# Kernel tuning notes

Measured on AMD Instinct MI355X. Metric: run time of the kernel, lower is better.

The kernel has to match this reference:

```python
import jax, jax.numpy as jnp
import numpy as np

N = 8192
DEGREE = 32          # fixed out-degree -> nnz(adj) = N*DEGREE, static for jit
NEG_SLOPE = 0.2      # GATConv default leaky_relu slope


def _gat_conv(x, src, dst, w, att_src, att_dst, b):
    """PyG GATConv (concat=True): x:[N,Fin], w:[Fin,H*C], att_*:[H,C], b:[H*C]."""
    n = x.shape[0]
    H, C = att_src.shape
    xl = (x @ w).reshape(n, H, C)                       # [N,H,C]
    a_s = jnp.einsum('nhc,hc->nh', xl, att_src)         # [N,H]
    a_d = jnp.einsum('nhc,hc->nh', xl, att_dst)         # [N,H]
    e = a_s[src] + a_d[dst]                             # [E,H]
    e = jnp.where(e > 0, e, NEG_SLOPE * e)              # leaky_relu
    # segment softmax over edges grouped by destination node
    m = jax.ops.segment_max(e, dst, num_segments=n)     # [N,H]
    ex = jnp.exp(e - m[dst])
    s = jax.ops.segment_sum(ex, dst, num_segments=n)    # [N,H]
    alpha = ex / s[dst]                                 # [E,H]
    out = jax.ops.segment_sum(alpha[:, :, None] * xl[src], dst, num_segments=n)
    return out.reshape(n, H * C) + b, alpha


def setup_inputs() -> dict:
    IN, HID, OUT, H = 256, 128, 64, 8
    key = jax.random.key(0)
    ks = jax.random.split(key, 12)

    x = jax.random.normal(ks[0], (N, IN), jnp.float32)

    # regular adjacency: node i -> (i+o) % N for o in 1..DEGREE (exactly N*DEGREE nonzeros)
    rows = jnp.repeat(jnp.arange(N), DEGREE)
    cols = ((jnp.arange(N)[:, None] + jnp.arange(1, DEGREE + 1)[None, :]) % N).reshape(-1)
    adj = jnp.zeros((N, N), jnp.float32).at[rows, cols].set(1.0)

    def glorot(k, shape):
        fan_in = shape[0] if len(shape) > 1 else shape[0]
        return jax.random.normal(k, shape, jnp.float32) * np.float32(1.0 / np.sqrt(fan_in))

    inp = {
        'x': x, 'adj': adj,
        'emb_w': glorot(ks[1], (IN, HID)), 'emb_b': jnp.zeros((HID,), jnp.float32),
        'w1': glorot(ks[2], (HID, H * HID)),
        'att_src1': jax.random.normal(ks[3], (H, HID), jnp.float32) * 0.1,
        'att_dst1': jax.random.normal(ks[4], (H, HID), jnp.float32) * 0.1,
        'b1': jnp.zeros((H * HID,), jnp.float32),
        'w2': glorot(ks[5], (H * HID, H * OUT)),
        'att_src2': jax.random.normal(ks[6], (H, OUT), jnp.float32) * 0.1,
        'att_dst2': jax.random.normal(ks[7], (H, OUT), jnp.float32) * 0.1,
        'b2': jnp.zeros((H * OUT,), jnp.float32),
    }
    return inp


def reference(x, adj, emb_w, emb_b, w1, att_src1, att_dst1, b1,
              w2, att_src2, att_dst2, b2):
    n = adj.shape[0]
    # dense_to_sparse: static nnz = N*DEGREE (by construction of adj)
    src, dst = jnp.nonzero(adj, size=n * DEGREE)
    h = x @ emb_w + emb_b                       # self.emb (dropout = identity in eval)
    h, _ = _gat_conv(h, src, dst, w1, att_src1, att_dst1, b1)
    h = jax.nn.relu(h)
    h, att = _gat_conv(h, src, dst, w2, att_src2, att_dst2, b2)
    h = jax.nn.relu(h)
    return h, att
```

## Files before the change

### kernel.cpp

```cpp
#include <hip/hip_runtime.h>
#include <hip/hip_bf16.h>

#define NN 8192
#define DEG 32

#define AS1 __attribute__((address_space(1)))
#define AS3 __attribute__((address_space(3)))

typedef unsigned short ushort_t;
typedef __attribute__((ext_vector_type(8))) short bf16x8;
typedef __attribute__((ext_vector_type(4))) float f32x4;

__device__ inline float bf_raw(unsigned short u) {
  return __uint_as_float(((unsigned int)u) << 16);
}
__device__ inline unsigned short f32_to_bf16_bits(float f) {
  __hip_bfloat16 b = __float2bfloat16(f);
  unsigned short u;
  __builtin_memcpy(&u, &b, sizeof(u));
  return u;
}
__device__ inline unsigned int pack2bf(float a, float b) {
  return (unsigned int)f32_to_bf16_bits(a) |
         ((unsigned int)f32_to_bf16_bits(b) << 16);
}

__device__ inline int detect_bf16(const unsigned int* __restrict__ raw) {
  __shared__ int s_cnt[4];
  int t = threadIdx.x;
  unsigned int w = raw[t];
  unsigned short lo = (unsigned short)(w & 0xffffu);
  int e = (lo >> 7) & 0xff;
  int ok = (lo == 0) || (e >= 96 && e <= 131);
  unsigned long long b = __ballot(ok);
  if ((t & 63) == 0) s_cnt[t >> 6] = __popcll(b);
  __syncthreads();
  int cnt = s_cnt[0] + s_cnt[1] + s_cnt[2] + s_cnt[3];
  __syncthreads();
  return cnt >= 145;
}

__device__ inline void tile_transpose64(const void* __restrict__ src,
                                        ushort_t* __restrict__ dst, int R,
                                        int C, int r0, int c0, int bf) {
  __shared__ float tile[64][65];
  int t = threadIdx.x;
  int cc = t & 63, rr = t >> 6;
#pragma unroll
  for (int p = 0; p < 16; ++p) {
    int r = p * 4 + rr;
    float v = bf ? bf_raw(((const ushort_t*)src)[(size_t)(r0 + r) * C + c0 + cc])
                 : ((const float*)src)[(size_t)(r0 + r) * C + c0 + cc];
    tile[r][cc] = v;
  }
  __syncthreads();
#pragma unroll
  for (int p = 0; p < 16; ++p) {
    int i = p * 4 + rr;
    dst[(size_t)(c0 + i) * R + r0 + cc] = f32_to_bf16_bits(tile[cc][i]);
  }
}

struct PrepArgs {
  const void* w2_raw;
  const void* embw_raw;
  const void* w1_raw;
  const void* embb_raw;
  ushort_t* w2t;
  ushort_t* W12t;
  float* b12;
  int* bfflag;
  const unsigned int* det;
};

__global__ __launch_bounds__(256) void prep_kernel(PrepArgs a) {
  int bf = detect_bf16(a.det);
  int b = blockIdx.x, t = threadIdx.x;
  if (b == 0 && t == 0) *a.bfflag = bf;
  if (b < 128) {
    tile_transpose64(a.w2_raw, a.w2t, 1024, 512, (b >> 3) * 64, (b & 7) * 64,
                     bf);
  } else {
    __shared__ float wcol[4][128];
    __shared__ float ebb[128];
    int idx = b - 128;
    int n0 = idx * 4;
    for (int i = t; i < 512; i += 256) {
      int n = i >> 7, j = i & 127;
      wcol[n][j] =
          bf ? bf_raw(((const ushort_t*)a.w1_raw)[(size_t)j * 1024 + n0 + n])
             : ((const float*)a.w1_raw)[(size_t)j * 1024 + n0 + n];
    }
    if (t < 128)
      ebb[t] = bf ? bf_raw(((const ushort_t*)a.embb_raw)[t])
                  : ((const float*)a.embb_raw)[t];
    __syncthreads();
    int k = t;
    float acc0 = 0.f, acc1 = 0.f, acc2 = 0.f, acc3 = 0.f;
#pragma unroll 4
    for (int jc = 0; jc < 16; ++jc) {
      float v[8];
      if (bf) {
        ushort4 u0 = ((const ushort4*)a.embw_raw)[k * 32 + jc * 2];
        ushort4 u1 = ((const ushort4*)a.embw_raw)[k * 32 + jc * 2 + 1];
        v[0] = bf_raw(u0.x); v[1] = bf_raw(u0.y);
        v[2] = bf_raw(u0.z); v[3] = bf_raw(u0.w);
        v[4] = bf_raw(u1.x); v[5] = bf_raw(u1.y);
        v[6] = bf_raw(u1.z); v[7] = bf_raw(u1.w);
      } else {
        float4 f0 = ((const float4*)a.embw_raw)[k * 32 + jc * 2];
        float4 f1 = ((const float4*)a.embw_raw)[k * 32 + jc * 2 + 1];
        v[0] = f0.x; v[1] = f0.y; v[2] = f0.z; v[3] = f0.w;
        v[4] = f1.x; v[5] = f1.y; v[6] = f1.z; v[7] = f1.w;
      }
#pragma unroll
      for (int jj = 0; jj < 8; ++jj) {
        acc0 = fmaf(v[jj], wcol[0][jc * 8 + jj], acc0);
        acc1 = fmaf(v[jj], wcol[1][jc * 8 + jj], acc1);
        acc2 = fmaf(v[jj], wcol[2][jc * 8 + jj], acc2);
        acc3 = fmaf(v[jj], wcol[3][jc * 8 + jj], acc3);
      }
    }
    a.W12t[(size_t)(n0 + 0) * 256 + k] = f32_to_bf16_bits(acc0);
    a.W12t[(size_t)(n0 + 1) * 256 + k] = f32_to_bf16_bits(acc1);
    a.W12t[(size_t)(n0 + 2) * 256 + k] = f32_to_bf16_bits(acc2);
    a.W12t[(size_t)(n0 + 3) * 256 + k] = f32_to_bf16_bits(acc3);
    int wv = t >> 6, ln = t & 63;
    float s = fmaf(ebb[ln], wcol[wv][ln], ebb[ln + 64] * wcol[wv][ln + 64]);
#pragma unroll
    for (int m = 1; m <= 32; m <<= 1) s += __shfl_xor(s, m);
    if (ln == 0) a.b12[n0 + wv] = s;
  }
}

template <int HPB, bool BIAS, bool ACHECK>
__global__ __launch_bounds__(512) void gemm_bt(
    const void* __restrict__ Araw, const ushort_t* __restrict__ Bt,
    const float* __restrict__ bias, ushort_t* __restrict__ C,
    const void* __restrict__ atts_raw, const void* __restrict__ attd_raw,
    float* __restrict__ a_s, float* __restrict__ a_d,
    const int* __restrict__ bfflag, int M, int N, int K) {
  __shared__ ushort_t As[128 * 64];
  __shared__ ushort_t Bs[128 * 64];
  __shared__ float ps[4][128], pd[4][128];
  int bf = bfflag[0];
  int abf = ACHECK ? bf : 1;
  int t = threadIdx.x;
  int wave = t >> 6, lane = t & 63;
  int wr = wave >> 2, wc = wave & 3;
  int wm = wr * 64, wn = wc * 32;
  int row0 = blockIdx.y * 128, col0 = blockIdx.x * 128;
  int q = lane >> 4, lr = lane & 15;
  int srow = t >> 3;
  int schunk = t & 7;

  int sc = (schunk ^ (srow & 7)) * 8;
  const ushort_t* gA0 = (const ushort_t*)Araw + (size_t)(row0 + srow) * K + sc;
  const ushort_t* gA1 =
      (const ushort_t*)Araw + (size_t)(row0 + 64 + srow) * K + sc;
  const float* fA0 = (const float*)Araw + (size_t)(row0 + srow) * K + sc;
  const float* fA1 = (const float*)Araw + (size_t)(row0 + 64 + srow) * K + sc;
  const ushort_t* gB0 = Bt + (size_t)(col0 + srow) * K + sc;
  const ushort_t* gB1 = Bt + (size_t)(col0 + 64 + srow) * K + sc;
  ushort_t* lA0 = As + srow * 64 + schunk * 8;
  ushort_t* lA1 = As + (64 + srow) * 64 + schunk * 8;
  ushort_t* lB0 = Bs + srow * 64 + schunk * 8;
  ushort_t* lB1 = Bs + (64 + srow) * 64 + schunk * 8;

  f32x4 acc[4][2];
#pragma unroll
  for (int i = 0; i < 4; ++i)
#pragma unroll
    for (int j = 0; j < 2; ++j)
#pragma unroll
      for (int r = 0; r < 4; ++r) acc[i][j][r] = 0.f;

  for (int k0 = 0; k0 < K; k0 += 64) {
    if (abf) {
      __builtin_amdgcn_global_load_lds((const AS1 void*)(gA0 + k0),
                                       (AS3 void*)lA0, 16, 0, 0);
      __builtin_amdgcn_global_load_lds((const AS1 void*)(gA1 + k0),
                                       (AS3 void*)lA1, 16, 0, 0);
    } else {
      float4 u0 = *(const float4*)(fA0 + k0);
      float4 u1 = *(const float4*)(fA0 + k0 + 4);
      uint4 o;
      o.x = pack2bf(u0.x, u0.y);
      o.y = pack2bf(u0.z, u0.w);
      o.z = pack2bf(u1.x, u1.y);
      o.w = pack2bf(u1.z, u1.w);
      *(uint4*)lA0 = o;
      u0 = *(const float4*)(fA1 + k0);
      u1 = *(const float4*)(fA1 + k0 + 4);
      o.x = pack2bf(u0.x, u0.y);
      o.y = pack2bf(u0.z, u0.w);
      o.z = pack2bf(u1.x, u1.y);
      o.w = pack2bf(u1.z, u1.w);
      *(uint4*)lA1 = o;
    }
    __builtin_amdgcn_global_load_lds((const AS1 void*)(gB0 + k0),
                                     (AS3 void*)lB0, 16, 0, 0);
    __builtin_amdgcn_global_load_lds((const AS1 void*)(gB1 + k0),
                                     (AS3 void*)lB1, 16, 0, 0);
    __syncthreads();
#pragma unroll
    for (int kk = 0; kk < 2; ++kk) {
      bf16x8 af[4], bfr[2];
#pragma unroll
      for (int i = 0; i < 4; ++i) {
        int r = wm + i * 16 + lr;
        int ci = kk * 4 + q;
        af[i] = *(const bf16x8*)(As + r * 64 + ((ci ^ (r & 7)) * 8));
      }
#pragma unroll
      for (int j = 0; j < 2; ++j) {
        int r = wn + j * 16 + lr;
        int ci = kk * 4 + q;
        bfr[j] = *(const bf16x8*)(Bs + r * 64 + ((ci ^ (r & 7)) * 8));
      }
#pragma unroll
      for (int i = 0; i < 4; ++i)
#pragma unroll
        for (int j = 0; j < 2; ++j)
          acc[i][j] = __builtin_amdgcn_mfma_f32_16x16x32_bf16(af[i], bfr[j],
                                                              acc[i][j], 0, 0, 0);
    }
    __syncthreads();
  }

#pragma unroll
  for (int i = 0; i < 4; ++i) {
#pragma unroll
    for (int j = 0; j < 2; ++j) {
      int col = col0 + wn + j * 16 + lr;
      float bv = BIAS ? bias[col] : 0.f;
#pragma unroll
      for (int rg = 0; rg < 4; ++rg) {
        int row = row0 + wm + i * 16 + q * 4 + rg;
        C[(size_t)row * N + col] = f32_to_bf16_bits(acc[i][j][rg] + bv);
      }
    }
  }

  float asv[2], adv[2];
#pragma unroll
  for (int j = 0; j < 2; ++j) {
    int col = col0 + wn + j * 16 + lr;
    asv[j] = bf ? bf_raw(((const ushort_t*)atts_raw)[col])
                : ((const float*)atts_raw)[col];
    adv[j] = bf ? bf_raw(((const ushort_t*)attd_raw)[col])
                : ((const float*)attd_raw)[col];
  }
#pragma unroll
  for (int i = 0; i < 4; ++i) {
#pragma unroll
    for (int rg = 0; rg < 4; ++rg) {
      float ls = fmaf(acc[i][0][rg], asv[0], acc[i][1][rg] * asv[1]);
      float ld = fmaf(acc[i][0][rg], adv[0], acc[i][1][rg] * adv[1]);
#pragma unroll
      for (int m = 1; m <= 8; m <<= 1) {
        ls += __shfl_xor(ls, m);
        ld += __shfl_xor(ld, m);
      }
      if (lr == 0) {
        int rl = wm + i * 16 + q * 4 + rg;
        ps[wc][rl] = ls;
        pd[wc][rl] = ld;
      }
    }
  }
  __syncthreads();
  if (HPB == 1) {
    if (t < 128) {
      a_s[(size_t)(row0 + t) * 8 + blockIdx.x] =
          ps[0][t] + ps[1][t] + ps[2][t] + ps[3][t];
      a_d[(size_t)(row0 + t) * 8 + blockIdx.x] =
          pd[0][t] + pd[1][t] + pd[2][t] + pd[3][t];
    }
  } else {
    if (t < 256) {
      int w = t >> 7, rl = t & 127;
      a_s[(size_t)(row0 + rl) * 8 + blockIdx.x * 2 + w] =
          ps[2 * w][rl] + ps[2 * w + 1][rl];
      a_d[(size_t)(row0 + rl) * 8 + blockIdx.x * 2 + w] =
          pd[2 * w][rl] + pd[2 * w + 1][rl];
    }
  }
}

__global__ __launch_bounds__(256) void attn1_kernel(
    const ushort_t* __restrict__ xl1, const float* __restrict__ a_s,
    const float* __restrict__ a_d, const void* __restrict__ b1raw,
    ushort_t* __restrict__ h1, const int* __restrict__ bfflag) {
  int bf = bfflag[0];
  int d0 = blockIdx.x * 8, t = threadIdx.x;
  __shared__ float sA[8][8][32];
  __shared__ ushort_t rows[39 * 128];
  int h = t >> 5, oo = t & 31;
#pragma unroll
  for (int dd = 0; dd < 8; ++dd) {
    int d = d0 + dd;
    int src = (d - (oo + 1)) & (NN - 1);
    float e = a_s[src * 8 + h] + a_d[d * 8 + h];
    e = e > 0.f ? e : 0.2f * e;
    float m = e;
#pragma unroll
    for (int k = 16; k >= 1; k >>= 1) m = fmaxf(m, __shfl_xor(m, k));
    float ex = __expf(e - m);
    float s = ex;
#pragma unroll
    for (int k = 16; k >= 1; k >>= 1) s += __shfl_xor(s, k);
    sA[dd][h][oo] = ex / s;
  }
  int dd = t >> 5, cq = t & 31;
  for (int f0 = 0; f0 < 1024; f0 += 128) {
    __syncthreads();
    for (int i = t; i < 39 * 16; i += 256) {
      int r = i >> 4, c8 = i & 15;
      int node = (d0 - 32 + r) & (NN - 1);
      __builtin_amdgcn_global_load_lds(
          (const AS1 void*)(xl1 + (size_t)node * 1024 + f0 + c8 * 8),
          (AS3 void*)(rows + r * 128 + c8 * 8), 16, 0, 0);
    }
    __syncthreads();
    int f = f0 + cq * 4;
    const float* al = sA[dd][f >> 7];
    float a0 = 0.f, a1 = 0.f, a2 = 0.f, a3 = 0.f;
#pragma unroll
    for (int o = 0; o < 32; ++o) {
      float a = al[o];
      ushort4 v = *(const ushort4*)(rows + (31 + dd - o) * 128 + cq * 4);
      a0 = fmaf(a, bf_raw(v.x), a0);
      a1 = fmaf(a, bf_raw(v.y), a1);
      a2 = fmaf(a, bf_raw(v.z), a2);
      a3 = fmaf(a, bf_raw(v.w), a3);
    }
    float4 bv;
    if (bf) {
      ushort4 ub = *(const ushort4*)((const ushort_t*)b1raw + f);
      bv.x = bf_raw(ub.x); bv.y = bf_raw(ub.y);
      bv.z = bf_raw(ub.z); bv.w = bf_raw(ub.w);
    } else {
      bv = *(const float4*)((const float*)b1raw + f);
    }
    ushort4 ov;
    ov.x = f32_to_bf16_bits(fmaxf(a0 + bv.x, 0.f));
    ov.y = f32_to_bf16_bits(fmaxf(a1 + bv.y, 0.f));
    ov.z = f32_to_bf16_bits(fmaxf(a2 + bv.z, 0.f));
    ov.w = f32_to_bf16_bits(fmaxf(a3 + bv.w, 0.f));
    *(ushort4*)(h1 + (size_t)(d0 + dd) * 1024 + f) = ov;
  }
}

__global__ __launch_bounds__(256) void attn2_kernel(
    const ushort_t* __restrict__ xl2, const float* __restrict__ a_s,
    const float* __restrict__ a_d, const void* __restrict__ b2raw,
    void* __restrict__ d_out, const int* __restrict__ bfflag) {
  int bf = bfflag[0];
  int d0 = blockIdx.x * 8, t = threadIdx.x;
  __shared__ float sA[8][8][32];
  __shared__ ushort_t rows[39 * 128];
  int h = t >> 5, oo = t & 31, o = oo + 1;
#pragma unroll
  for (int dd = 0; dd < 8; ++dd) {
    int d = d0 + dd;
    int src = (d - o) & (NN - 1);
    float e = a_s[src * 8 + h] + a_d[d * 8 + h];
    e = e > 0.f ? e : 0.2f * e;
    float m = e;
#pragma unroll
    for (int k = 16; k >= 1; k >>= 1) m = fmaxf(m, __shfl_xor(m, k));
    float ex = __expf(e - m);
    float s = ex;
#pragma unroll
    for (int k = 16; k >= 1; k >>= 1) s += __shfl_xor(s, k);
    float alpha = ex / s;
    sA[dd][h][oo] = alpha;
    int W = src + 33 - NN;
    if (W < 0) W = 0;
    int rank = (src > d) ? d : (W + o - 1);
    size_t aidx = (size_t)NN * 512 + ((size_t)src * DEG + rank) * 8 + h;
    if (bf)
      ((ushort_t*)d_out)[aidx] = f32_to_bf16_bits(alpha);
    else
      ((float*)d_out)[aidx] = alpha;
  }
  int dd = t >> 5, cq = t & 31;
  for (int f0 = 0; f0 < 512; f0 += 128) {
    __syncthreads();
    for (int i = t; i < 39 * 16; i += 256) {
      int r = i >> 4, c8 = i & 15;
      int node = (d0 - 32 + r) & (NN - 1);
      __builtin_amdgcn_global_load_lds(
          (const AS1 void*)(xl2 + (size_t)node * 512 + f0 + c8 * 8),
          (AS3 void*)(rows + r * 128 + c8 * 8), 16, 0, 0);
    }
    __syncthreads();
    int f = f0 + cq * 4;
    const float* al = sA[dd][f >> 6];
    float a0 = 0.f, a1 = 0.f, a2 = 0.f, a3 = 0.f;
#pragma unroll
    for (int oi = 0; oi < 32; ++oi) {
      float a = al[oi];
      ushort4 v = *(const ushort4*)(rows + (31 + dd - oi) * 128 + cq * 4);
      a0 = fmaf(a, bf_raw(v.x), a0);
      a1 = fmaf(a, bf_raw(v.y), a1);
      a2 = fmaf(a, bf_raw(v.z), a2);
      a3 = fmaf(a, bf_raw(v.w), a3);
    }
    float4 bv;
    if (bf) {
      ushort4 ub = *(const ushort4*)((const ushort_t*)b2raw + f);
      bv.x = bf_raw(ub.x); bv.y = bf_raw(ub.y);
      bv.z = bf_raw(ub.z); bv.w = bf_raw(ub.w);
    } else {
      bv = *(const float4*)((const float*)b2raw + f);
    }
    float v0 = fmaxf(a0 + bv.x, 0.f), v1 = fmaxf(a1 + bv.y, 0.f);
    float v2 = fmaxf(a2 + bv.z, 0.f), v3 = fmaxf(a3 + bv.w, 0.f);
    size_t hidx = (size_t)(d0 + dd) * 512 + f;
    if (bf) {
      ushort4 ov;
      ov.x = f32_to_bf16_bits(v0);
      ov.y = f32_to_bf16_bits(v1);
      ov.z = f32_to_bf16_bits(v2);
      ov.w = f32_to_bf16_bits(v3);
      *(ushort4*)((ushort_t*)d_out + hidx) = ov;
    } else {
      float4 ov = {v0, v1, v2, v3};
      *(float4*)((float*)d_out + hidx) = ov;
    }
  }
}

extern "C" void kernel_launch(void* const* d_in, const int* in_sizes, int n_in,
                              void* d_out, int out_size, void* d_ws,
                              size_t ws_size, hipStream_t stream) {
  char* wsb = (char*)d_ws;
  size_t off = 0;
  auto alloc = [&](size_t bytes) {
    char* p = wsb + off;
    off += (bytes + 255) & ~(size_t)255;
    return p;
  };
  ushort_t* w2t   = (ushort_t*)alloc((size_t)512 * 1024 * 2);
  ushort_t* W12t  = (ushort_t*)alloc((size_t)1024 * 256 * 2);
  float* b12  = (float*)alloc(1024 * 4);
  int* bfp    = (int*)alloc(256);
  float* a_s1 = (float*)alloc((size_t)NN * 8 * 4);
  float* a_d1 = (float*)alloc((size_t)NN * 8 * 4);
  float* a_s2 = (float*)alloc((size_t)NN * 8 * 4);
  float* a_d2 = (float*)alloc((size_t)NN * 8 * 4);
  ushort_t* xl1 = (ushort_t*)alloc((size_t)NN * 1024 * 2);
  ushort_t* h1  = (ushort_t*)alloc((size_t)NN * 1024 * 2);
  ushort_t* xl2 = xl1;
  if (ws_size < off) return;

  PrepArgs a;
  a.w2_raw = d_in[8];
  a.embw_raw = d_in[2];
  a.w1_raw = d_in[4];
  a.embb_raw = d_in[3];
  a.w2t = w2t;
  a.W12t = W12t;
  a.b12 = b12;
  a.bfflag = bfp;
  a.det = (const unsigned int*)d_in[5];

  prep_kernel<<<128 + 256, 256, 0, stream>>>(a);

  gemm_bt<1, true, true><<<dim3(8, 64), 512, 0, stream>>>(
      d_in[0], W12t, b12, xl1, d_in[5], d_in[6], a_s1, a_d1, bfp, NN, 1024,
      256);
  attn1_kernel<<<NN / 8, 256, 0, stream>>>(xl1, a_s1, a_d1, d_in[7], h1, bfp);
  gemm_bt<2, false, false><<<dim3(4, 64), 512, 0, stream>>>(
      h1, w2t, nullptr, xl2, d_in[9], d_in[10], a_s2, a_d2, bfp, NN, 512,
      1024);
  attn2_kernel<<<NN / 8, 256, 0, stream>>>(xl2, a_s2, a_d2, d_in[11], d_out,
                                           bfp);
}
```

Before: 420.5 us.

## Pre-convert x to bf16 in prep and retile second GEMM to 128x64 blocks

The fp32-to-bf16 conversion of x moves into the prep kernel as a separate elementwise pass, so the first GEMM always streams A through direct global-to-LDS loads instead of converting in registers. The second GEMM becomes its own kernel with 128x64 tiles, 256 threads and a flat 512-block grid, doubling the block count to fill the CUs better. This costs an extra pass over x (read fp32, write bf16) and more redundant reads of the A tile in GEMM2.

```diff
diff --git a/kernel.cpp b/kernel.cpp
--- a/kernel.cpp
+++ b/kernel.cpp
@@ -62,10 +62,12 @@
 }
 
 struct PrepArgs {
+  const void* x_raw;
   const void* w2_raw;
   const void* embw_raw;
   const void* w1_raw;
   const void* embb_raw;
+  ushort_t* xc;
   ushort_t* w2t;
   ushort_t* W12t;
   float* b12;
@@ -77,13 +79,27 @@
   int bf = detect_bf16(a.det);
   int b = blockIdx.x, t = threadIdx.x;
   if (b == 0 && t == 0) *a.bfflag = bf;
-  if (b < 128) {
-    tile_transpose64(a.w2_raw, a.w2t, 1024, 512, (b >> 3) * 64, (b & 7) * 64,
-                     bf);
+  if (b < 2048) {
+    int i = b * 256 + t;
+    if (bf) {
+      ((ushort4*)a.xc)[i] = ((const ushort4*)a.x_raw)[i];
+    } else {
+      float4 v = ((const float4*)a.x_raw)[i];
+      ushort4 o;
+      o.x = f32_to_bf16_bits(v.x);
+      o.y = f32_to_bf16_bits(v.y);
+      o.z = f32_to_bf16_bits(v.z);
+      o.w = f32_to_bf16_bits(v.w);
+      ((ushort4*)a.xc)[i] = o;
+    }
+  } else if (b < 2048 + 128) {
+    int idx = b - 2048;
+    tile_transpose64(a.w2_raw, a.w2t, 1024, 512, (idx >> 3) * 64,
+                     (idx & 7) * 64, bf);
   } else {
     __shared__ float wcol[4][128];
     __shared__ float ebb[128];
-    int idx = b - 128;
+    int idx = b - (2048 + 128);
     int n0 = idx * 4;
     for (int i = t; i < 512; i += 256) {
       int n = i >> 7, j = i & 127;
@@ -133,33 +149,27 @@
   }
 }
 
-template <int HPB, bool BIAS, bool ACHECK>
-__global__ __launch_bounds__(512) void gemm_bt(
-    const void* __restrict__ Araw, const ushort_t* __restrict__ Bt,
+__global__ __launch_bounds__(512) void gemm1_kernel(
+    const ushort_t* __restrict__ A, const ushort_t* __restrict__ Bt,
     const float* __restrict__ bias, ushort_t* __restrict__ C,
     const void* __restrict__ atts_raw, const void* __restrict__ attd_raw,
     float* __restrict__ a_s, float* __restrict__ a_d,
-    const int* __restrict__ bfflag, int M, int N, int K) {
+    const int* __restrict__ bfflag, int N, int K) {
   __shared__ ushort_t As[128 * 64];
   __shared__ ushort_t Bs[128 * 64];
   __shared__ float ps[4][128], pd[4][128];
   int bf = bfflag[0];
-  int abf = ACHECK ? bf : 1;
   int t = threadIdx.x;
   int wave = t >> 6, lane = t & 63;
   int wr = wave >> 2, wc = wave & 3;
   int wm = wr * 64, wn = wc * 32;
   int row0 = blockIdx.y * 128, col0 = blockIdx.x * 128;
   int q = lane >> 4, lr = lane & 15;
-  int srow = t >> 3;
-  int schunk = t & 7;
+  int srow = t >> 3, schunk = t & 7;
 
   int sc = (schunk ^ (srow & 7)) * 8;
-  const ushort_t* gA0 = (const ushort_t*)Araw + (size_t)(row0 + srow) * K + sc;
-  const ushort_t* gA1 =
-      (const ushort_t*)Araw + (size_t)(row0 + 64 + srow) * K + sc;
-  const float* fA0 = (const float*)Araw + (size_t)(row0 + srow) * K + sc;
-  const float* fA1 = (const float*)Araw + (size_t)(row0 + 64 + srow) * K + sc;
+  const ushort_t* gA0 = A + (size_t)(row0 + srow) * K + sc;
+  const ushort_t* gA1 = A + (size_t)(row0 + 64 + srow) * K + sc;
   const ushort_t* gB0 = Bt + (size_t)(col0 + srow) * K + sc;
   const ushort_t* gB1 = Bt + (size_t)(col0 + 64 + srow) * K + sc;
   ushort_t* lA0 = As + srow * 64 + schunk * 8;
@@ -176,28 +186,10 @@
       for (int r = 0; r < 4; ++r) acc[i][j][r] = 0.f;
 
   for (int k0 = 0; k0 < K; k0 += 64) {
-    if (abf) {
-      __builtin_amdgcn_global_load_lds((const AS1 void*)(gA0 + k0),
-                                       (AS3 void*)lA0, 16, 0, 0);
-      __builtin_amdgcn_global_load_lds((const AS1 void*)(gA1 + k0),
-                                       (AS3 void*)lA1, 16, 0, 0);
-    } else {
-      float4 u0 = *(const float4*)(fA0 + k0);
-      float4 u1 = *(const float4*)(fA0 + k0 + 4);
-      uint4 o;
-      o.x = pack2bf(u0.x, u0.y);
-      o.y = pack2bf(u0.z, u0.w);
-      o.z = pack2bf(u1.x, u1.y);
-      o.w = pack2bf(u1.z, u1.w);
-      *(uint4*)lA0 = o;
-      u0 = *(const float4*)(fA1 + k0);
-      u1 = *(const float4*)(fA1 + k0 + 4);
-      o.x = pack2bf(u0.x, u0.y);
-      o.y = pack2bf(u0.z, u0.w);
-      o.z = pack2bf(u1.x, u1.y);
-      o.w = pack2bf(u1.z, u1.w);
-      *(uint4*)lA1 = o;
-    }
+    __builtin_amdgcn_global_load_lds((const AS1 void*)(gA0 + k0),
+                                     (AS3 void*)lA0, 16, 0, 0);
+    __builtin_amdgcn_global_load_lds((const AS1 void*)(gA1 + k0),
+                                     (AS3 void*)lA1, 16, 0, 0);
     __builtin_amdgcn_global_load_lds((const AS1 void*)(gB0 + k0),
                                      (AS3 void*)lB0, 16, 0, 0);
     __builtin_amdgcn_global_load_lds((const AS1 void*)(gB1 + k0),
@@ -233,7 +225,7 @@
 #pragma unroll
     for (int j = 0; j < 2; ++j) {
       int col = col0 + wn + j * 16 + lr;
-      float bv = BIAS ? bias[col] : 0.f;
+      float bv = bias[col];
 #pragma unroll
       for (int rg = 0; rg < 4; ++rg) {
         int row = row0 + wm + i * 16 + q * 4 + rg;
@@ -270,21 +262,123 @@
     }
   }
   __syncthreads();
-  if (HPB == 1) {
-    if (t < 128) {
-      a_s[(size_t)(row0 + t) * 8 + blockIdx.x] =
-          ps[0][t] + ps[1][t] + ps[2][t] + ps[3][t];
-      a_d[(size_t)(row0 + t) * 8 + blockIdx.x] =
-          pd[0][t] + pd[1][t] + pd[2][t] + pd[3][t];
-    }
-  } else {
-    if (t < 256) {
-      int w = t >> 7, rl = t & 127;
-      a_s[(size_t)(row0 + rl) * 8 + blockIdx.x * 2 + w] =
-          ps[2 * w][rl] + ps[2 * w + 1][rl];
-      a_d[(size_t)(row0 + rl) * 8 + blockIdx.x * 2 + w] =
-          pd[2 * w][rl] + pd[2 * w + 1][rl];
-    }
+  if (t < 128) {
+    a_s[(size_t)(row0 + t) * 8 + blockIdx.x] =
+        ps[0][t] + ps[1][t] + ps[2][t] + ps[3][t];
+    a_d[(size_t)(row0 + t) * 8 + blockIdx.x] =
+        pd[0][t] + pd[1][t] + pd[2][t] + pd[3][t];
+  }
+}
+
+__global__ __launch_bounds__(256) void gemm2_kernel(
+    const ushort_t* __restrict__ A, const ushort_t* __restrict__ Bt,
+    ushort_t* __restrict__ C, const void* __restrict__ atts_raw,
+    const void* __restrict__ attd_raw, float* __restrict__ a_s,
+    float* __restrict__ a_d, const int* __restrict__ bfflag, int N, int K) {
+  __shared__ ushort_t As[128 * 64];
+  __shared__ ushort_t Bs[64 * 64];
+  __shared__ float ps[2][128], pd[2][128];
+  int bf = bfflag[0];
+  int t = threadIdx.x;
+  int ux = blockIdx.x & 7, uy = blockIdx.x >> 3;
+  int wave = t >> 6, lane = t & 63;
+  int wr = wave >> 1, wc = wave & 1;
+  int wm = wr * 64, wn = wc * 32;
+  int row0 = uy * 128, col0 = ux * 64;
+  int q = lane >> 4, lr = lane & 15;
+  int srow = t >> 3, schunk = t & 7;
+  int sc = (schunk ^ (srow & 7)) * 8;
+  const ushort_t* gA = A + (size_t)(row0 + srow) * K + sc;
+  const ushort_t* gB = Bt + (size_t)(col0 + srow) * K + sc;
+  ushort_t* lA = As + srow * 64 + schunk * 8;
+  ushort_t* lB = Bs + srow * 64 + schunk * 8;
+
+  f32x4 acc[4][2];
+#pragma unroll
+  for (int i = 0; i < 4; ++i)
+#pragma unroll
+    for (int j = 0; j < 2; ++j)
+#pragma unroll
+      for (int r = 0; r < 4; ++r) acc[i][j][r] = 0.f;
+
+  for (int k0 = 0; k0 < K; k0 += 64) {
+#pragma unroll
+    for (int rr = 0; rr < 4; ++rr)
+      __builtin_amdgcn_global_load_lds(
+          (const AS1 void*)(gA + (size_t)(rr * 32) * K + k0),
+          (AS3 void*)(lA + rr * 32 * 64), 16, 0, 0);
+#pragma unroll
+    for (int rr = 0; rr < 2; ++rr)
+      __builtin_amdgcn_global_load_lds(
+          (const AS1 void*)(gB + (size_t)(rr * 32) * K + k0),
+          (AS3 void*)(lB + rr * 32 * 64), 16, 0, 0);
+    __syncthreads();
+#pragma unroll
+    for (int kk = 0; kk < 2; ++kk) {
+      bf16x8 af[4], bfr[2];
+      int ci = kk * 4 + q;
+#pragma unroll
+      for (int i = 0; i < 4; ++i) {
+        int r = wm + i * 16 + lr;
+        af[i] = *(const bf16x8*)(As + r * 64 + ((ci ^ (r & 7)) * 8));
+      }
+#pragma unroll
+      for (int j = 0; j < 2; ++j) {
+        int r = wn + j * 16 + lr;
+        bfr[j] = *(const bf16x8*)(Bs + r * 64 + ((ci ^ (r & 7)) * 8));
+      }
+#pragma unroll
+      for (int i = 0; i < 4; ++i)
+#pragma unroll
+        for (int j = 0; j < 2; ++j)
+          acc[i][j] = __builtin_amdgcn_mfma_f32_16x16x32_bf16(af[i], bfr[j],
+                                                              acc[i][j], 0, 0, 0);
+    }
+    __syncthreads();
+  }
+
+#pragma unroll
+  for (int i = 0; i < 4; ++i)
+#pragma unroll
+    for (int j = 0; j < 2; ++j) {
+      int col = col0 + wn + j * 16 + lr;
+#pragma unroll
+      for (int rg = 0; rg < 4; ++rg) {
+        int row = row0 + wm + i * 16 + q * 4 + rg;
+        C[(size_t)row * N + col] = f32_to_bf16_bits(acc[i][j][rg]);
+      }
+    }
+
+  float asv[2], adv[2];
+#pragma unroll
+  for (int j = 0; j < 2; ++j) {
+    int col = col0 + wn + j * 16 + lr;
+    asv[j] = bf ? bf_raw(((const ushort_t*)atts_raw)[col])
+                : ((const float*)atts_raw)[col];
+    adv[j] = bf ? bf_raw(((const ushort_t*)attd_raw)[col])
+                : ((const float*)attd_raw)[col];
+  }
+#pragma unroll
+  for (int i = 0; i < 4; ++i)
+#pragma unroll
+    for (int rg = 0; rg < 4; ++rg) {
+      float ls = fmaf(acc[i][0][rg], asv[0], acc[i][1][rg] * asv[1]);
+      float ld = fmaf(acc[i][0][rg], adv[0], acc[i][1][rg] * adv[1]);
+#pragma unroll
+      for (int mm = 1; mm <= 8; mm <<= 1) {
+        ls += __shfl_xor(ls, mm);
+        ld += __shfl_xor(ld, mm);
+      }
+      if (lr == 0) {
+        int rl = wm + i * 16 + q * 4 + rg;
+        ps[wc][rl] = ls;
+        pd[wc][rl] = ld;
+      }
+    }
+  __syncthreads();
+  if (t < 128) {
+    a_s[(size_t)(row0 + t) * 8 + ux] = ps[0][t] + ps[1][t];
+    a_d[(size_t)(row0 + t) * 8 + ux] = pd[0][t] + pd[1][t];
   }
 }
 
@@ -443,6 +537,7 @@
     off += (bytes + 255) & ~(size_t)255;
     return p;
   };
+  ushort_t* xc    = (ushort_t*)alloc((size_t)NN * 256 * 2);
   ushort_t* w2t   = (ushort_t*)alloc((size_t)512 * 1024 * 2);
   ushort_t* W12t  = (ushort_t*)alloc((size_t)1024 * 256 * 2);
   float* b12  = (float*)alloc(1024 * 4);
@@ -457,25 +552,25 @@
   if (ws_size < off) return;
 
   PrepArgs a;
+  a.x_raw = d_in[0];
   a.w2_raw = d_in[8];
   a.embw_raw = d_in[2];
   a.w1_raw = d_in[4];
   a.embb_raw = d_in[3];
+  a.xc = xc;
   a.w2t = w2t;
   a.W12t = W12t;
   a.b12 = b12;
   a.bfflag = bfp;
   a.det = (const unsigned int*)d_in[5];
 
-  prep_kernel<<<128 + 256, 256, 0, stream>>>(a);
-
-  gemm_bt<1, true, true><<<dim3(8, 64), 512, 0, stream>>>(
-      d_in[0], W12t, b12, xl1, d_in[5], d_in[6], a_s1, a_d1, bfp, NN, 1024,
-      256);
+  prep_kernel<<<2048 + 128 + 256, 256, 0, stream>>>(a);
+
+  gemm1_kernel<<<dim3(8, 64), 512, 0, stream>>>(
+      xc, W12t, b12, xl1, d_in[5], d_in[6], a_s1, a_d1, bfp, 1024, 256);
   attn1_kernel<<<NN / 8, 256, 0, stream>>>(xl1, a_s1, a_d1, d_in[7], h1, bfp);
-  gemm_bt<2, false, false><<<dim3(4, 64), 512, 0, stream>>>(
-      h1, w2t, nullptr, xl2, d_in[9], d_in[10], a_s2, a_d2, bfp, NN, 512,
-      1024);
+  gemm2_kernel<<<512, 256, 0, stream>>>(h1, w2t, xl2, d_in[9], d_in[10], a_s2,
+                                        a_d2, bfp, 512, 1024);
   attn2_kernel<<<NN / 8, 256, 0, stream>>>(xl2, a_s2, a_d2, d_in[11], d_out,
                                            bfp);
 }
```

Result: no change. 418.5 us (-0.5%).
